# Kernel optimization log

Measured on AMD Instinct MI355X. Metric: run time of the kernel, lower is better.

Reference implementation:

```python
import jax, jax.numpy as jnp
import numpy as np

B, L, D, H = 4, 1024, 256, 8
TEMP = float(np.sqrt(D))
EPS_SM = 1e-6
EPS_LN = 1e-5


def setup_inputs() -> dict:
    key = jax.random.key(0)
    ks = jax.random.split(key, 8)
    std = float(np.sqrt(2.0 / (D * 2)))
    return {
        "q": jax.random.normal(ks[0], (B, L, D), jnp.float32),
        "mask": jax.random.randint(ks[1], (B, L, L), 0, 2, jnp.int32),
        "k": jax.random.normal(ks[2], (B, L, D), jnp.float32),
        "v": jax.random.normal(ks[3], (B, L, D), jnp.float32),
        "w_qs": jax.random.normal(ks[4], (H * D, D), jnp.float32) * std,
        "w_ks": jax.random.normal(ks[5], (H * D, D), jnp.float32) * std,
        "w_vs": jax.random.normal(ks[6], (H * D, D), jnp.float32) * std,
        "fc_w": jax.random.normal(ks[7], (D, H * D), jnp.float32) * float(np.sqrt(2.0 / (D + H * D))),
        "fc_b": jnp.zeros((D,), jnp.float32),
        "ln_g": jnp.ones((D,), jnp.float32),
        "ln_b": jnp.zeros((D,), jnp.float32),
    }


def masked_softmax(x, m):
    # repo's layers.masked_softmax: clamp, mask-mul, stable exp, mask-mul, normalize
    x = jnp.clip(x, -15.0, 15.0) * m
    e = jnp.exp(x - jnp.max(x, axis=-1, keepdims=True)) * m
    return e / (jnp.sum(e, axis=-1, keepdims=True) + EPS_SM)


def reference(q, mask, k, v, w_qs, w_ks, w_vs, fc_w, fc_b, ln_g, ln_b):
    residual = q
    m = mask.astype(q.dtype)[:, None, :, :]          # [B,1,Lq,Lk]
    # projections to per-head full-dim: [B,L,H,D]
    qh = (q @ w_qs.T).reshape(B, L, H, D)
    kh = (k @ w_ks.T).reshape(B, L, H, D)
    vh = (v @ w_vs.T).reshape(B, L, H, D)
    scores = jnp.einsum("bqhd,bkhd->bhqk", qh, kh) / TEMP   # [B,H,Lq,Lk]
    attn = masked_softmax(scores, m)
    out = jnp.einsum("bhqk,bkhd->bqhd", attn, vh).reshape(B, L, H * D)
    out = out @ fc_w.T + fc_b                         # [B,L,D]
    out = out + residual
    mu = jnp.mean(out, axis=-1, keepdims=True)
    var = jnp.var(out, axis=-1, keepdims=True)
    out = (out - mu) / jnp.sqrt(var + EPS_LN) * ln_g + ln_b
    # match torch attn layout: [H*B, Lq, Lk] (head-major)
    attn_hb = jnp.transpose(attn, (1, 0, 2, 3)).reshape(H * B, L, L)
    return out, attn_hb
```

## Files before the change

kernel.cpp:

```cpp
#include <hip/hip_runtime.h>
#include <cstdint>
#include <math.h>

#define Bsz 4
#define Lsz 1024
#define Dsz 256
#define Hsz 8
#define HD  2048
#define NROWS (Bsz*Lsz)
#define INV_TEMP 0.0625f

typedef __attribute__((ext_vector_type(8))) short bf16x8;
typedef __attribute__((ext_vector_type(4))) float f32x4;

__device__ inline unsigned short f2bf(float f) {
    union { float f; unsigned u; } x; x.f = f;
    unsigned r = x.u + 0x7fffu + ((x.u >> 16) & 1u);
    return (unsigned short)(r >> 16);
}
__device__ inline float bf2f(unsigned short u) {
    union { unsigned u; float f; } x; x.u = (unsigned)u << 16; return x.f;
}

#define GBL(p) ((const __attribute__((address_space(1))) unsigned int*)(p))
#define LDS(p) ((__attribute__((address_space(3))) unsigned int*)(p))

template <int TMv, int TNv, typename OutT, int EPI, int MINW, int DB>
__global__ __launch_bounds__(256, MINW) void gemm_bt(
    const unsigned short* __restrict__ A, const unsigned short* __restrict__ Bm,
    OutT* __restrict__ C,
    int K, int lda, int ldb, int ldc, int inner,
    long long sA1, long long sA2, long long sB1, long long sB2,
    long long sC1, long long sC2, float alpha,
    const unsigned short* __restrict__ maskb, long long sM2,
    const float* __restrict__ invs, long long sI1, long long sI2,
    float* __restrict__ aux)
{
    constexpr int WMv = TMv / 2, WNv = TNv / 2;
    constexpr int IT = TMv / 32, JT = TNv / 32;
    constexpr int APASS = TMv / 32, NPASS = (TMv + TNv) / 32;
    constexpr int TILE = (TMv + TNv) * 64;

    const int z  = blockIdx.z;
    const int i1 = z / inner;
    const int i2 = z % inner;
    A  += (size_t)i1 * sA1 + (size_t)i2 * sA2;
    Bm += (size_t)i1 * sB1 + (size_t)i2 * sB2;
    C  += (size_t)i1 * sC1 + (size_t)i2 * sC2;
    if (EPI == 1) { maskb += (size_t)i2 * sM2; aux += (size_t)z * Lsz; }
    if (EPI == 2) { invs  += (size_t)i1 * sI1 + (size_t)i2 * sI2; aux += (size_t)z * Lsz * Lsz; }

    __shared__ unsigned short S[(DB ? 2 : 1) * TILE];
    __shared__ float inv_lds[EPI == 2 ? TMv : 1];

    const int t    = threadIdx.x;
    const int lane = t & 63;
    const int w    = t >> 6;
    const int wm   = w & 1;
    const int wn   = w >> 1;
    const int m0   = blockIdx.x * TMv;
    const int n0   = blockIdx.y * TNv;

    const int rA = t >> 3;
    const int ch = ((t & 7) ^ (rA & 7)) * 8;
    const unsigned short* gA = A  + (size_t)(m0 + rA) * lda + ch;
    const unsigned short* gB = Bm + (size_t)(n0 + rA) * ldb + ch;

    const int fr = lane & 15;
    const int q  = lane >> 4;

    f32x4 acc[IT][JT];
#pragma unroll
    for (int i = 0; i < IT; ++i)
#pragma unroll
        for (int j = 0; j < JT; ++j) acc[i][j] = (f32x4){0.f, 0.f, 0.f, 0.f};

    auto stage = [&](unsigned short* Sb, int k0) {
#pragma unroll
        for (int p = 0; p < NPASS; ++p) {
            const unsigned short* src = (p < APASS)
                ? (gA + (size_t)p * 32 * lda + k0)
                : (gB + (size_t)(p - APASS) * 32 * ldb + k0);
            __builtin_amdgcn_global_load_lds(GBL(src), LDS(Sb + p * 2048 + t * 8), 16, 0, 0);
        }
    };
    auto kstep = [&](const unsigned short* As) {
        const unsigned short* Bs = As + TMv * 64;
#pragma unroll
        for (int ks = 0; ks < 2; ++ks) {
            const int slot = ((ks * 4 + q) ^ (fr & 7)) * 8;
            bf16x8 a[IT], b[JT];
#pragma unroll
            for (int i = 0; i < IT; ++i)
                a[i] = *(const bf16x8*)(As + (wm * WMv + i * 16 + fr) * 64 + slot);
#pragma unroll
            for (int j = 0; j < JT; ++j)
                b[j] = *(const bf16x8*)(Bs + (wn * WNv + j * 16 + fr) * 64 + slot);
#pragma unroll
            for (int i = 0; i < IT; ++i)
#pragma unroll
                for (int j = 0; j < JT; ++j)
                    acc[i][j] = __builtin_amdgcn_mfma_f32_16x16x32_bf16(a[i], b[j], acc[i][j], 0, 0, 0);
        }
    };

    if constexpr (EPI == 2) {
        if (t < TMv) inv_lds[t] = 1.0f / (invs[m0 + t] + 1e-6f);
    }

    if constexpr (DB) {
        const int nk = K >> 6;
        stage(S, 0);
        __syncthreads();
        int cur = 0;
        for (int kt = 0; kt < nk; ++kt) {
            if (kt + 1 < nk) stage(S + (cur ^ 1) * TILE, (kt + 1) << 6);
            kstep(S + cur * TILE);
            if constexpr (EPI == 2) {
                if ((kt >= (nk >> 1)) == (blockIdx.y == 1)) {
                    const unsigned short* As = S + cur * TILE;
                    const int chunk = lane & 7;
                    const int rsub  = lane >> 3;
#pragma unroll
                    for (int pass = 0; pass < TMv / 32; ++pass) {
                        const int row = w * (TMv / 4) + pass * 8 + rsub;
                        const uint4 u = *(const uint4*)(As + row * 64 + ((chunk ^ (row & 7)) * 8));
                        const float iv = inv_lds[row];
                        float4 lo, hi;
                        lo.x = bf2f((unsigned short)(u.x & 0xffff)) * iv; lo.y = bf2f((unsigned short)(u.x >> 16)) * iv;
                        lo.z = bf2f((unsigned short)(u.y & 0xffff)) * iv; lo.w = bf2f((unsigned short)(u.y >> 16)) * iv;
                        hi.x = bf2f((unsigned short)(u.z & 0xffff)) * iv; hi.y = bf2f((unsigned short)(u.z >> 16)) * iv;
                        hi.z = bf2f((unsigned short)(u.w & 0xffff)) * iv; hi.w = bf2f((unsigned short)(u.w >> 16)) * iv;
                        float* op = aux + (size_t)(m0 + row) * Lsz + (kt << 6) + chunk * 8;
                        *(float4*)op = lo;
                        *(float4*)(op + 4) = hi;
                    }
                }
            }
            __syncthreads();
            cur ^= 1;
        }
    } else {
        for (int k0 = 0; k0 < K; k0 += 64) {
            stage(S, k0);
            __syncthreads();
            kstep(S);
            __syncthreads();
        }
    }

#pragma unroll
    for (int i = 0; i < IT; ++i) {
#pragma unroll
        for (int r = 0; r < 4; ++r) {
            const int row = m0 + wm * WMv + i * 16 + q * 4 + r;
            float rsum = 0.f;
#pragma unroll
            for (int j = 0; j < JT; ++j) {
                const int col = n0 + wn * WNv + j * 16 + fr;
                float vv = acc[i][j][r] * alpha;
                if (EPI == 0) {
                    if constexpr (sizeof(OutT) == 4)
                        C[(size_t)row * ldc + col] = (OutT)vv;
                    else
                        ((unsigned short*)C)[(size_t)row * ldc + col] = f2bf(vv);
                } else if (EPI == 1) {
                    const float m = bf2f(maskb[(size_t)row * Lsz + col]);
                    vv = fminf(fmaxf(vv, -15.f), 15.f) * m;
                    vv = __expf(vv) * m;
                    const unsigned short us = f2bf(vv);
                    ((unsigned short*)C)[(size_t)row * ldc + col] = us;
                    rsum += bf2f(us);
                } else {
                    vv *= inv_lds[row - m0];
                    ((unsigned short*)C)[(size_t)row * ldc + col] = f2bf(vv);
                }
            }
            if constexpr (EPI == 1) {
#pragma unroll
                for (int o = 1; o <= 8; o <<= 1) rsum += __shfl_xor(rsum, o, 64);
                if (fr == 0) atomicAdd(&aux[row], rsum);
            }
        }
    }
}

__global__ __launch_bounds__(256) void cast_all(
    const float* __restrict__ q, const float* __restrict__ k, const float* __restrict__ v,
    const float* __restrict__ wq, const float* __restrict__ wk, const float* __restrict__ wv,
    const float* __restrict__ fw, const int* __restrict__ mask,
    unsigned short* __restrict__ qb, unsigned short* __restrict__ kb, unsigned short* __restrict__ vb,
    unsigned short* __restrict__ wqb, unsigned short* __restrict__ wkb, unsigned short* __restrict__ wvb,
    unsigned short* __restrict__ fwb, unsigned short* __restrict__ mb,
    float* __restrict__ rs)
{
    const int gid = blockIdx.x * 256 + threadIdx.x;
    const int NQ = 262144;
    const int NW = 131072;
    const int NF = 3 * NQ + 4 * NW;
    const int NM = 1048576;
    if (gid >= NF) {
        const int off = gid - NF;
        if (off >= NM) {
            const int ri = off - NM;
            if (ri < 8192) ((float4*)rs)[ri] = (float4){0.f, 0.f, 0.f, 0.f};
            return;
        }
        const int4 mi = ((const int4*)mask)[off];
        ushort4 o;
        o.x = mi.x ? 0x3F80 : 0;
        o.y = mi.y ? 0x3F80 : 0;
        o.z = mi.z ? 0x3F80 : 0;
        o.w = mi.w ? 0x3F80 : 0;
        ((ushort4*)mb)[off] = o;
        return;
    }
    const float* src; unsigned short* dst; int off;
    if      (gid < NQ)            { src = q;  dst = qb;  off = gid; }
    else if (gid < 2 * NQ)        { src = k;  dst = kb;  off = gid - NQ; }
    else if (gid < 3 * NQ)        { src = v;  dst = vb;  off = gid - 2 * NQ; }
    else if (gid < 3 * NQ + NW)   { src = wq; dst = wqb; off = gid - 3 * NQ; }
    else if (gid < 3 * NQ + 2*NW) { src = wk; dst = wkb; off = gid - 3 * NQ - NW; }
    else if (gid < 3 * NQ + 3*NW) { src = wv; dst = wvb; off = gid - 3 * NQ - 2 * NW; }
    else                          { src = fw; dst = fwb; off = gid - 3 * NQ - 3 * NW; }
    float4 f = ((const float4*)src)[off];
    ushort4 o;
    o.x = f2bf(f.x); o.y = f2bf(f.y); o.z = f2bf(f.z); o.w = f2bf(f.w);
    ((ushort4*)dst)[off] = o;
}

__global__ __launch_bounds__(256) void ln_kernel(const float* __restrict__ gout,
                                                 const float* __restrict__ qin,
                                                 const float* __restrict__ fc_b,
                                                 const float* __restrict__ ln_g,
                                                 const float* __restrict__ ln_b,
                                                 float* __restrict__ out)
{
    const int row = blockIdx.x;
    const int t = threadIdx.x;
    const size_t idx = (size_t)row * Dsz + t;
    const size_t P = (size_t)NROWS * Dsz;
    const float val = gout[idx] + gout[idx + P] + gout[idx + 2 * P] + gout[idx + 3 * P]
                    + fc_b[t] + qin[idx];

    __shared__ float red[4];
    float s = val;
#pragma unroll
    for (int o = 32; o > 0; o >>= 1) s += __shfl_down(s, o, 64);
    const int lane = t & 63, w = t >> 6;
    if (lane == 0) red[w] = s;
    __syncthreads();
    const float mu = (red[0] + red[1] + red[2] + red[3]) * (1.0f / Dsz);
    __syncthreads();

    float d = val - mu;
    float s2 = d * d;
#pragma unroll
    for (int o = 32; o > 0; o >>= 1) s2 += __shfl_down(s2, o, 64);
    if (lane == 0) red[w] = s2;
    __syncthreads();
    const float var = (red[0] + red[1] + red[2] + red[3]) * (1.0f / Dsz);

    out[idx] = d * rsqrtf(var + 1e-5f) * ln_g[t] + ln_b[t];
}

extern "C" void kernel_launch(void* const* d_in, const int* in_sizes, int n_in,
                              void* d_out, int out_size, void* d_ws, size_t ws_size,
                              hipStream_t stream)
{
    const float* q    = (const float*)d_in[0];
    const int*   mask = (const int*)d_in[1];
    const float* k    = (const float*)d_in[2];
    const float* v    = (const float*)d_in[3];
    const float* w_qs = (const float*)d_in[4];
    const float* w_ks = (const float*)d_in[5];
    const float* w_vs = (const float*)d_in[6];
    const float* fc_w = (const float*)d_in[7];
    const float* fc_b = (const float*)d_in[8];
    const float* ln_g = (const float*)d_in[9];
    const float* ln_b = (const float*)d_in[10];

    float* out  = (float*)d_out;
    float* attn = (float*)d_out + (size_t)NROWS * Dsz;

    unsigned short* wsu = (unsigned short*)d_ws;
    unsigned short* qh     = wsu;
    unsigned short* kh     = qh + (size_t)NROWS * HD;
    unsigned short* q_bf   = kh + (size_t)NROWS * HD;
    unsigned short* k_bf   = q_bf + (size_t)NROWS * Dsz;
    unsigned short* v_bf   = k_bf + (size_t)NROWS * Dsz;
    unsigned short* wq_bf  = v_bf + (size_t)NROWS * Dsz;
    unsigned short* wk_bf  = wq_bf + (size_t)HD * Dsz;
    unsigned short* wv_bf  = wk_bf + (size_t)HD * Dsz;
    unsigned short* vt     = wv_bf + (size_t)HD * Dsz;
    unsigned short* attn_e = vt + (size_t)Bsz * HD * Lsz;
    unsigned short* attnv  = attn_e + (size_t)32 * Lsz * Lsz;
    unsigned short* fcw_bf = attnv + (size_t)NROWS * HD;
    float*          rowsum = (float*)(fcw_bf + (size_t)Dsz * HD);
    float*          fcout  = rowsum + 32768;
    unsigned short* maskb  = (unsigned short*)(fcout + (size_t)4 * NROWS * Dsz);

    dim3 blk(256);

    cast_all<<<dim3(9248), blk, 0, stream>>>(q, k, v, w_qs, w_ks, w_vs, fc_w, mask,
                                             q_bf, k_bf, v_bf, wq_bf, wk_bf, wv_bf, fcw_bf, maskb,
                                             rowsum);

    {
        dim3 grid(NROWS / 128, HD / 128, 2);
        gemm_bt<128, 128, unsigned short, 0, 3, 0><<<grid, blk, 0, stream>>>(q_bf, wq_bf, qh,
            Dsz, Dsz, Dsz, HD, 2,
            0, (long long)NROWS * Dsz, 0, (long long)HD * Dsz, 0, (long long)NROWS * HD,
            1.0f, nullptr, 0, nullptr, 0, 0, nullptr);
    }

    {
        dim3 grid(HD / 128, Lsz / 128, Bsz);
        gemm_bt<128, 128, unsigned short, 0, 2, 1><<<grid, blk, 0, stream>>>(wv_bf, v_bf, vt,
            Dsz, Dsz, Dsz, Lsz, 1,
            0, 0, (long long)Lsz * Dsz, 0, (long long)HD * Lsz, 0,
            1.0f, nullptr, 0, nullptr, 0, 0, nullptr);
    }

    {
        dim3 grid(Lsz / 128, Lsz / 128, Hsz * Bsz);
        gemm_bt<128, 128, unsigned short, 1, 3, 0><<<grid, blk, 0, stream>>>(qh, kh, attn_e,
            Dsz, HD, HD, Lsz, Bsz,
            Dsz, (long long)Lsz * HD, Dsz, (long long)Lsz * HD,
            (long long)Bsz * Lsz * Lsz, (long long)Lsz * Lsz,
            INV_TEMP, maskb, (long long)Lsz * Lsz, nullptr, 0, 0, rowsum);
    }

    {
        dim3 grid(Lsz / 64, Dsz / 128, Hsz * Bsz);
        gemm_bt<64, 128, unsigned short, 2, 3, 1><<<grid, blk, 0, stream>>>(attn_e, vt, attnv,
            Lsz, Lsz, Lsz, HD, Bsz,
            (long long)Bsz * Lsz * Lsz, (long long)Lsz * Lsz,
            (long long)Dsz * Lsz, (long long)HD * Lsz,
            Dsz, (long long)Lsz * HD,
            1.0f, nullptr, 0, rowsum, (long long)Bsz * Lsz, (long long)Lsz, attn);
    }

    {
        dim3 grid(NROWS / 64, Dsz / 128, 4);
        gemm_bt<64, 128, float, 0, 3, 1><<<grid, blk, 0, stream>>>(attnv, fcw_bf, fcout,
            512, HD, HD, Dsz, 4,
            0, 512, 0, 512, 0, (long long)NROWS * Dsz,
            1.0f, nullptr, 0, nullptr, 0, 0, nullptr);
    }

    ln_kernel<<<dim3(NROWS), blk, 0, stream>>>(fcout, q, fc_b, ln_g, ln_b, out);
}
```

Before: 337.6 us.

## Unify GEMMs on double-buffered pipeline with explicit vmcnt waits and 64x128 tiles

Removes the single-buffer path and makes every GEMM use a double-buffered LDS pipeline. Full __syncthreads are replaced by hand-written s_waitcnt vmcnt/lgkmcnt plus raw s_barrier, so the next tile's global loads can stay in flight while the current tile is computed. The projection and score GEMMs move from 128x128 to 64x128 tiles, giving more blocks and occupancy at the cost of less reuse per block. The vmcnt literals assume exactly six loads per stage plus the epilogue stores, which makes the code fragile if the compiler reorders or splits memory operations.

Result: no change. 335.6 us (-0.6%).

```diff
diff --git a/kernel.cpp b/kernel.cpp
--- a/kernel.cpp
+++ b/kernel.cpp
@@ -25,7 +25,7 @@
 #define GBL(p) ((const __attribute__((address_space(1))) unsigned int*)(p))
 #define LDS(p) ((__attribute__((address_space(3))) unsigned int*)(p))
 
-template <int TMv, int TNv, typename OutT, int EPI, int MINW, int DB>
+template <int TMv, int TNv, typename OutT, int EPI, int MINW>
 __global__ __launch_bounds__(256, MINW) void gemm_bt(
     const unsigned short* __restrict__ A, const unsigned short* __restrict__ Bm,
     OutT* __restrict__ C,
@@ -40,6 +40,7 @@
     constexpr int IT = TMv / 32, JT = TNv / 32;
     constexpr int APASS = TMv / 32, NPASS = (TMv + TNv) / 32;
     constexpr int TILE = (TMv + TNv) * 64;
+    static_assert(NPASS == 6, "vmcnt literals below assume NPASS==6");
 
     const int z  = blockIdx.z;
     const int i1 = z / inner;
@@ -50,7 +51,7 @@
     if (EPI == 1) { maskb += (size_t)i2 * sM2; aux += (size_t)z * Lsz; }
     if (EPI == 2) { invs  += (size_t)i1 * sI1 + (size_t)i2 * sI2; aux += (size_t)z * Lsz * Lsz; }
 
-    __shared__ unsigned short S[(DB ? 2 : 1) * TILE];
+    __shared__ unsigned short S[2 * TILE];
     __shared__ float inv_lds[EPI == 2 ? TMv : 1];
 
     const int t    = threadIdx.x;
@@ -104,49 +105,59 @@
         }
     };
 
+    const int nk = K >> 6;
+    const bool y1 = (blockIdx.y == 1);
+
+    stage(S, 0);
     if constexpr (EPI == 2) {
         if (t < TMv) inv_lds[t] = 1.0f / (invs[m0 + t] + 1e-6f);
-    }
-
-    if constexpr (DB) {
-        const int nk = K >> 6;
-        stage(S, 0);
         __syncthreads();
-        int cur = 0;
-        for (int kt = 0; kt < nk; ++kt) {
-            if (kt + 1 < nk) stage(S + (cur ^ 1) * TILE, (kt + 1) << 6);
-            kstep(S + cur * TILE);
-            if constexpr (EPI == 2) {
-                if ((kt >= (nk >> 1)) == (blockIdx.y == 1)) {
-                    const unsigned short* As = S + cur * TILE;
-                    const int chunk = lane & 7;
-                    const int rsub  = lane >> 3;
-#pragma unroll
-                    for (int pass = 0; pass < TMv / 32; ++pass) {
-                        const int row = w * (TMv / 4) + pass * 8 + rsub;
-                        const uint4 u = *(const uint4*)(As + row * 64 + ((chunk ^ (row & 7)) * 8));
-                        const float iv = inv_lds[row];
-                        float4 lo, hi;
-                        lo.x = bf2f((unsigned short)(u.x & 0xffff)) * iv; lo.y = bf2f((unsigned short)(u.x >> 16)) * iv;
-                        lo.z = bf2f((unsigned short)(u.y & 0xffff)) * iv; lo.w = bf2f((unsigned short)(u.y >> 16)) * iv;
-                        hi.x = bf2f((unsigned short)(u.z & 0xffff)) * iv; hi.y = bf2f((unsigned short)(u.z >> 16)) * iv;
-                        hi.z = bf2f((unsigned short)(u.w & 0xffff)) * iv; hi.w = bf2f((unsigned short)(u.w >> 16)) * iv;
-                        float* op = aux + (size_t)(m0 + row) * Lsz + (kt << 6) + chunk * 8;
-                        *(float4*)op = lo;
-                        *(float4*)(op + 4) = hi;
-                    }
+    }
+
+    for (int kt = 0; kt < nk; ++kt) {
+        if (kt + 1 < nk) stage(S + ((kt + 1) & 1) * TILE, (kt + 1) << 6);
+
+        if constexpr (EPI == 2) {
+            const bool pstore = (kt >= 1) && (((kt - 1) >= (nk >> 1)) == y1);
+            if (kt + 1 < nk) {
+                if (pstore) asm volatile("s_waitcnt vmcnt(10)" ::: "memory");
+                else        asm volatile("s_waitcnt vmcnt(6)"  ::: "memory");
+            } else {
+                if (pstore) asm volatile("s_waitcnt vmcnt(4)"  ::: "memory");
+                else        asm volatile("s_waitcnt vmcnt(0)"  ::: "memory");
+            }
+        } else {
+            if (kt + 1 < nk) asm volatile("s_waitcnt vmcnt(6)" ::: "memory");
+            else             asm volatile("s_waitcnt vmcnt(0)" ::: "memory");
+        }
+        __builtin_amdgcn_s_barrier();
+
+        kstep(S + (kt & 1) * TILE);
+
+        if constexpr (EPI == 2) {
+            if ((kt >= (nk >> 1)) == y1) {
+                const unsigned short* As = S + (kt & 1) * TILE;
+                const int chunk = lane & 7;
+                const int rsub  = lane >> 3;
+#pragma unroll
+                for (int pass = 0; pass < TMv / 32; ++pass) {
+                    const int row = w * (TMv / 4) + pass * 8 + rsub;
+                    const uint4 u = *(const uint4*)(As + row * 64 + ((chunk ^ (row & 7)) * 8));
+                    const float iv = inv_lds[row];
+                    float4 lo, hi;
+                    lo.x = bf2f((unsigned short)(u.x & 0xffff)) * iv; lo.y = bf2f((unsigned short)(u.x >> 16)) * iv;
+                    lo.z = bf2f((unsigned short)(u.y & 0xffff)) * iv; lo.w = bf2f((unsigned short)(u.y >> 16)) * iv;
+                    hi.x = bf2f((unsigned short)(u.z & 0xffff)) * iv; hi.y = bf2f((unsigned short)(u.z >> 16)) * iv;
+                    hi.z = bf2f((unsigned short)(u.w & 0xffff)) * iv; hi.w = bf2f((unsigned short)(u.w >> 16)) * iv;
+                    float* op = aux + (size_t)(m0 + row) * Lsz + (kt << 6) + chunk * 8;
+                    *(float4*)op = lo;
+                    *(float4*)(op + 4) = hi;
                 }
             }
-            __syncthreads();
-            cur ^= 1;
-        }
-    } else {
-        for (int k0 = 0; k0 < K; k0 += 64) {
-            stage(S, k0);
-            __syncthreads();
-            kstep(S);
-            __syncthreads();
-        }
+        }
+
+        asm volatile("s_waitcnt lgkmcnt(0)" ::: "memory");
+        __builtin_amdgcn_s_barrier();
     }
 
 #pragma unroll
@@ -307,24 +318,24 @@
                                              rowsum);
 
     {
-        dim3 grid(NROWS / 128, HD / 128, 2);
-        gemm_bt<128, 128, unsigned short, 0, 3, 0><<<grid, blk, 0, stream>>>(q_bf, wq_bf, qh,
+        dim3 grid(NROWS / 64, HD / 128, 2);
+        gemm_bt<64, 128, unsigned short, 0, 3><<<grid, blk, 0, stream>>>(q_bf, wq_bf, qh,
             Dsz, Dsz, Dsz, HD, 2,
             0, (long long)NROWS * Dsz, 0, (long long)HD * Dsz, 0, (long long)NROWS * HD,
             1.0f, nullptr, 0, nullptr, 0, 0, nullptr);
     }
 
     {
-        dim3 grid(HD / 128, Lsz / 128, Bsz);
-        gemm_bt<128, 128, unsigned short, 0, 2, 1><<<grid, blk, 0, stream>>>(wv_bf, v_bf, vt,
+        dim3 grid(HD / 64, Lsz / 128, Bsz);
+        gemm_bt<64, 128, unsigned short, 0, 3><<<grid, blk, 0, stream>>>(wv_bf, v_bf, vt,
             Dsz, Dsz, Dsz, Lsz, 1,
             0, 0, (long long)Lsz * Dsz, 0, (long long)HD * Lsz, 0,
             1.0f, nullptr, 0, nullptr, 0, 0, nullptr);
     }
 
     {
-        dim3 grid(Lsz / 128, Lsz / 128, Hsz * Bsz);
-        gemm_bt<128, 128, unsigned short, 1, 3, 0><<<grid, blk, 0, stream>>>(qh, kh, attn_e,
+        dim3 grid(Lsz / 64, Lsz / 128, Hsz * Bsz);
+        gemm_bt<64, 128, unsigned short, 1, 3><<<grid, blk, 0, stream>>>(qh, kh, attn_e,
             Dsz, HD, HD, Lsz, Bsz,
             Dsz, (long long)Lsz * HD, Dsz, (long long)Lsz * HD,
             (long long)Bsz * Lsz * Lsz, (long long)Lsz * Lsz,
@@ -333,7 +344,7 @@
 
     {
         dim3 grid(Lsz / 64, Dsz / 128, Hsz * Bsz);
-        gemm_bt<64, 128, unsigned short, 2, 3, 1><<<grid, blk, 0, stream>>>(attn_e, vt, attnv,
+        gemm_bt<64, 128, unsigned short, 2, 3><<<grid, blk, 0, stream>>>(attn_e, vt, attnv,
             Lsz, Lsz, Lsz, HD, Bsz,
             (long long)Bsz * Lsz * Lsz, (long long)Lsz * Lsz,
             (long long)Dsz * Lsz, (long long)HD * Lsz,
@@ -343,7 +354,7 @@
 
     {
         dim3 grid(NROWS / 64, Dsz / 128, 4);
-        gemm_bt<64, 128, float, 0, 3, 1><<<grid, blk, 0, stream>>>(attnv, fcw_bf, fcout,
+        gemm_bt<64, 128, float, 0, 3><<<grid, blk, 0, stream>>>(attnv, fcw_bf, fcout,
             512, HD, HD, Dsz, 4,
             0, 512, 0, 512, 0, (long long)NROWS * Dsz,
             1.0f, nullptr, 0, nullptr, 0, 0, nullptr);
```
